# Kernel tuning notes

Hardware: AMD Instinct MI355X
Metric: run time of the kernel (lower is better)

The kernel has to match this reference:

```python
import jax, jax.numpy as jnp
import numpy as np

BUCKET_SIZE = 64  # init kwarg bucket_size
DIM = 64          # init kwarg dim (per-head dim, used for scaling)


def setup_inputs() -> dict:
    key = jax.random.key(0)
    kq, kk = jax.random.split(key)
    q = jax.random.normal(kq, (32, 8192, 64), dtype=jnp.float32)
    k = jax.random.normal(kk, (32, 8192, 64), dtype=jnp.float32)
    return {"q": q, "k": k}


def _cumavg(t):
    # cumulative average along the sequence axis (axis=1)
    r = jnp.arange(1, t.shape[1] + 1, dtype=t.dtype)
    return jnp.cumsum(t, axis=1) / r[None, :, None]


def reference(q, k):
    bh, n, d = q.shape
    buckets = n // BUCKET_SIZE
    kv_buckets = k.shape[1] // BUCKET_SIZE

    # bucket the cumulative averages: [bh, buckets, bucket_size, d]
    q_r = _cumavg(q).reshape(bh, buckets, BUCKET_SIZE, d)
    k_r = _cumavg(k).reshape(bh, kv_buckets, BUCKET_SIZE, d)

    sq = q_r[:, :, 0]                                   # [bh, buckets, d]
    sk = k_r.sum(axis=2)                                # [bh, kv_buckets, d]
    sk = jnp.pad(sk, ((0, 0), (1, 0), (0, 0)))          # pad one zero bucket row at front

    R = jnp.einsum('bie,bje->bij', sq, sk) * (DIM ** -0.5)  # [bh, buckets, kv_buckets+1]

    rows = jnp.arange(buckets)[:, None]
    cols = jnp.arange(kv_buckets + 1)[None, :]
    neg = -jnp.finfo(R.dtype).max
    # masked_fill: for row i, columns i+1..buckets set to -max (cols > rows)
    R = jnp.where(cols > rows, neg, R)
    R = jax.nn.softmax(R, axis=-1)
    # tril(diagonal=-1): keep entries with col < row
    R = jnp.where(cols < rows, R, jnp.zeros((), R.dtype))
    return R
```

## Files before the change

kernel.cpp:

```cpp
#include <hip/hip_runtime.h>
#include <cstddef>

constexpr int BH = 32;
constexpr int N  = 8192;
constexpr int D  = 64;
constexpr int BK = 64;
constexpr int NB = 128;
constexpr int NC = 129;

__global__ __launch_bounds__(256) void kA(const float* __restrict__ q,
                                          const float* __restrict__ k,
                                          float* __restrict__ qsum,
                                          float* __restrict__ ksum,
                                          float* __restrict__ kw,
                                          float* __restrict__ qfirst,
                                          float* __restrict__ W) {
  const int wv   = threadIdx.x >> 6;
  const int lane = threadIdx.x & 63;
  const int f    = lane & 15;
  const int r    = lane >> 4;
  const int j    = blockIdx.x * 4 + wv;
  const int b    = blockIdx.y;
  const int side = blockIdx.z;
  const int base = j * BK;
  const size_t ob = ((size_t)b * NB + j) * D;

  const float* src = (side == 0 ? q : k) + ((size_t)b * N + base) * D;
  const float4* s4 = (const float4*)src;

  if (side == 0) {
    float4 v[16];
#pragma unroll
    for (int p = 0; p < 16; ++p) v[p] = s4[(r * 16 + p) * 16 + f];

    float a[4] = {0, 0, 0, 0};
#pragma unroll
    for (int p = 0; p < 16; ++p) {
      a[0] += v[p].x; a[1] += v[p].y; a[2] += v[p].z; a[3] += v[p].w;
    }
#pragma unroll
    for (int c = 0; c < 4; ++c) {
      a[c] += __shfl_xor(a[c], 16, 64);
      a[c] += __shfl_xor(a[c], 32, 64);
    }
    if (r == 0) {
      ((float4*)(qsum + ob))[f] = make_float4(a[0], a[1], a[2], a[3]);
      ((float4*)(qfirst + ob))[f] = v[0];
    }
  } else {
    float4 v[16];
#pragma unroll
    for (int p = 0; p < 16; ++p) v[p] = s4[(r * 16 + 15 - p) * 16 + f];

    float ak[4] = {0, 0, 0, 0}, aw[4] = {0, 0, 0, 0};
    float wh = 0.0f;
#pragma unroll
    for (int p = 0; p < 16; ++p) {
      const int row = r * 16 + 15 - p;
      wh += 1.0f / (float)(base + row + 1);
      ak[0] += v[p].x; ak[1] += v[p].y; ak[2] += v[p].z; ak[3] += v[p].w;
      aw[0] += v[p].x * wh; aw[1] += v[p].y * wh;
      aw[2] += v[p].z * wh; aw[3] += v[p].w * wh;
    }

    const float w16 = __shfl_xor(wh, 16, 64);
    const float w32 = __shfl_xor(wh, 32, 64);
    const float w48 = __shfl_xor(wh, 48, 64);
    float TU = 0.0f;
    if ((r ^ 1) > r) TU += w16;
    if ((r ^ 2) > r) TU += w32;
    if ((r ^ 3) > r) TU += w48;
    const float Wfull = wh + w16 + w32 + w48;

#pragma unroll
    for (int c = 0; c < 4; ++c) aw[c] += TU * ak[c];
#pragma unroll
    for (int c = 0; c < 4; ++c) {
      ak[c] += __shfl_xor(ak[c], 16, 64); ak[c] += __shfl_xor(ak[c], 32, 64);
      aw[c] += __shfl_xor(aw[c], 16, 64); aw[c] += __shfl_xor(aw[c], 32, 64);
    }
    if (r == 0) {
      ((float4*)(ksum + ob))[f] = make_float4(ak[0], ak[1], ak[2], ak[3]);
      ((float4*)(kw   + ob))[f] = make_float4(aw[0], aw[1], aw[2], aw[3]);
      if (lane == 0 && b == 0) W[j] = Wfull;
    }
  }
}

__global__ __launch_bounds__(256) void kB(const float* __restrict__ qsum,
                                          const float* __restrict__ ksum,
                                          const float* __restrict__ kw,
                                          const float* __restrict__ qfirst,
                                          const float* __restrict__ W,
                                          float* __restrict__ sq,
                                          float* __restrict__ skp) {
  const int side = blockIdx.x;
  const int b    = blockIdx.y;
  const int tid  = threadIdx.x;
  const int d    = tid & 63;
  const int jg   = tid >> 6;

  __shared__ float buf[NB * D];
  __shared__ float tot[4 * D];
  __shared__ float Wl[NB];

  const float* src = (side == 0 ? qsum : ksum) + (size_t)b * NB * D;
  {
    const float4* g4 = (const float4*)src;
    float4* l4 = (float4*)buf;
    for (int u = tid; u < NB * D / 4; u += 256) l4[u] = g4[u];
    if (side == 1 && tid < NB) Wl[tid] = W[tid];
  }
  __syncthreads();

  float t0 = 0.0f;
  for (int jj = 0; jj < 32; ++jj) t0 += buf[(jg * 32 + jj) * D + d];
  tot[jg * D + d] = t0;
  __syncthreads();

  float pre = 0.0f;
  for (int g = 0; g < jg; ++g) pre += tot[g * D + d];

  if (side == 0) {
    for (int jj = 0; jj < 32; ++jj) {
      const int j = jg * 32 + jj;
      const size_t o = ((size_t)b * NB + j) * D + d;
      sq[o] = (pre + qfirst[o]) / (float)(j * BK + 1);
      pre += buf[j * D + d];
    }
  } else {
    if (tid < D) skp[(size_t)b * NC * D + tid] = 0.0f;
    for (int jj = 0; jj < 32; ++jj) {
      const int j = jg * 32 + jj;
      const size_t o = ((size_t)b * NB + j) * D + d;
      skp[((size_t)b * NC + j + 1) * D + d] = pre * Wl[j] + kw[o];
      pre += buf[j * D + d];
    }
  }
}

__global__ __launch_bounds__(256) void kC(const float* __restrict__ sq,
                                          const float* __restrict__ skp,
                                          float* __restrict__ out) {
  const int tile = blockIdx.x, b = blockIdx.y;
  const int tid = threadIdx.x;
  const int jp = tid & 63, rep = tid >> 6;
  const int T0 = tile * 8;
  const int rows = T0 + 8;

  __shared__ float skpS[NB * D];
  __shared__ float sqs[8 * D];

  {
    const float4* g4 = (const float4*)(skp + (size_t)b * NC * D);
    for (int u = tid; u < rows * 16; u += 256) {
      const int row = u >> 4, f = u & 15;
      ((float4*)skpS)[row * 16 + ((f + row) & 15)] = g4[u];
    }
    if (tid < 128)
      ((float4*)sqs)[tid] = ((const float4*)(sq + ((size_t)b * NB + T0) * D))[tid];
  }
  __syncthreads();

  float acc0[2] = {0, 0}, acc1[2] = {0, 0};
  const float4* sk4 = (const float4*)skpS;
  const float4* sq4 = (const float4*)sqs;
#pragma unroll
  for (int d4 = 0; d4 < 16; ++d4) {
    const int slot = (d4 + jp) & 15;
    const float4 k0 = sk4[jp * 16 + slot];
    const float4 k1 = sk4[(jp + 64) * 16 + slot];
#pragma unroll
    for (int ii = 0; ii < 2; ++ii) {
      const float4 s = sq4[(rep * 2 + ii) * 16 + d4];
      acc0[ii] += s.x * k0.x + s.y * k0.y + s.z * k0.z + s.w * k0.w;
      acc1[ii] += s.x * k1.x + s.y * k1.y + s.z * k1.z + s.w * k1.w;
    }
  }

#pragma unroll
  for (int ii = 0; ii < 2; ++ii) {
    const int i = T0 + rep * 2 + ii;
    const int j0 = jp, j1 = jp + 64;
    const float v0 = acc0[ii] * 0.125f, v1 = acc1[ii] * 0.125f;
    const bool val0 = (j0 <= i), val1 = (j1 <= i);
    float m = fmaxf(val0 ? v0 : -3.402823466e38f, val1 ? v1 : -3.402823466e38f);
#pragma unroll
    for (int s = 1; s < 64; s <<= 1) m = fmaxf(m, __shfl_xor(m, s, 64));
    const float e0 = val0 ? __expf(v0 - m) : 0.0f;
    const float e1 = val1 ? __expf(v1 - m) : 0.0f;
    float ss = e0 + e1;
#pragma unroll
    for (int s = 1; s < 64; s <<= 1) ss += __shfl_xor(ss, s, 64);
    const float rden = 1.0f / ss;
    float* orow = out + ((size_t)b * NB + i) * NC;
    orow[j0] = (j0 < i) ? e0 * rden : 0.0f;
    orow[j1] = (j1 < i) ? e1 * rden : 0.0f;
    if (jp == 0) orow[128] = 0.0f;
  }
}

extern "C" void kernel_launch(void* const* d_in, const int* in_sizes, int n_in,
                              void* d_out, int out_size, void* d_ws, size_t ws_size,
                              hipStream_t stream) {
  const float* q = (const float*)d_in[0];
  const float* k = (const float*)d_in[1];
  float* out = (float*)d_out;

  float* ws     = (float*)d_ws;
  float* qsum   = ws;
  float* ksum   = qsum   + (size_t)BH * NB * D;
  float* kw     = ksum   + (size_t)BH * NB * D;
  float* qfirst = kw     + (size_t)BH * NB * D;
  float* sq     = qfirst + (size_t)BH * NB * D;
  float* skp    = sq     + (size_t)BH * NB * D;
  float* W      = skp    + (size_t)BH * NC * D;

  kA<<<dim3(NB / 4, BH, 2), 256, 0, stream>>>(q, k, qsum, ksum, kw, qfirst, W);
  kB<<<dim3(2, BH), 256, 0, stream>>>(qsum, ksum, kw, qfirst, W, sq, skp);
  kC<<<dim3(16, BH), 256, 0, stream>>>(sq, skp, out);
}
```

Measured before the change: 160.6 us.

## Restructure bucket reduction kernel: one block per bucket handling both q and k

The first kernel now assigns one 256-thread block per (bucket, head) that loads both q and k rows, instead of one wavefront per bucket per side. The harmonic weight suffix sums are computed with a wave-level shuffle scan, and per-wave partials are combined through shared memory. The aim is more memory-level parallelism: each thread holds fewer float4 loads in flight and more blocks are spread across CUs. The cost is an extra shared-memory reduction and a barrier per block.

```diff
diff --git a/kernel.cpp b/kernel.cpp
--- a/kernel.cpp
+++ b/kernel.cpp
@@ -8,82 +8,74 @@
 constexpr int NB = 128;
 constexpr int NC = 129;
 
-__global__ __launch_bounds__(256) void kA(const float* __restrict__ q,
-                                          const float* __restrict__ k,
-                                          float* __restrict__ qsum,
-                                          float* __restrict__ ksum,
-                                          float* __restrict__ kw,
-                                          float* __restrict__ qfirst,
-                                          float* __restrict__ W) {
-  const int wv   = threadIdx.x >> 6;
-  const int lane = threadIdx.x & 63;
-  const int f    = lane & 15;
-  const int r    = lane >> 4;
-  const int j    = blockIdx.x * 4 + wv;
-  const int b    = blockIdx.y;
-  const int side = blockIdx.z;
+__global__ __launch_bounds__(256, 1) void kA(const float* __restrict__ q,
+                                             const float* __restrict__ k,
+                                             float* __restrict__ qsum,
+                                             float* __restrict__ ksum,
+                                             float* __restrict__ kw,
+                                             float* __restrict__ qfirst,
+                                             float* __restrict__ W) {
+  const int j = blockIdx.x, b = blockIdx.y;
+  const int tid  = threadIdx.x;
+  const int f    = tid & 15;
+  const int rr   = tid >> 4;
+  const int w    = tid >> 6;
+  const int lane = tid & 63;
   const int base = j * BK;
   const size_t ob = ((size_t)b * NB + j) * D;
 
-  const float* src = (side == 0 ? q : k) + ((size_t)b * N + base) * D;
-  const float4* s4 = (const float4*)src;
-
-  if (side == 0) {
-    float4 v[16];
-#pragma unroll
-    for (int p = 0; p < 16; ++p) v[p] = s4[(r * 16 + p) * 16 + f];
-
-    float a[4] = {0, 0, 0, 0};
-#pragma unroll
-    for (int p = 0; p < 16; ++p) {
-      a[0] += v[p].x; a[1] += v[p].y; a[2] += v[p].z; a[3] += v[p].w;
-    }
-#pragma unroll
-    for (int c = 0; c < 4; ++c) {
-      a[c] += __shfl_xor(a[c], 16, 64);
-      a[c] += __shfl_xor(a[c], 32, 64);
-    }
-    if (r == 0) {
-      ((float4*)(qsum + ob))[f] = make_float4(a[0], a[1], a[2], a[3]);
-      ((float4*)(qfirst + ob))[f] = v[0];
-    }
-  } else {
-    float4 v[16];
-#pragma unroll
-    for (int p = 0; p < 16; ++p) v[p] = s4[(r * 16 + 15 - p) * 16 + f];
-
-    float ak[4] = {0, 0, 0, 0}, aw[4] = {0, 0, 0, 0};
-    float wh = 0.0f;
-#pragma unroll
-    for (int p = 0; p < 16; ++p) {
-      const int row = r * 16 + 15 - p;
-      wh += 1.0f / (float)(base + row + 1);
-      ak[0] += v[p].x; ak[1] += v[p].y; ak[2] += v[p].z; ak[3] += v[p].w;
-      aw[0] += v[p].x * wh; aw[1] += v[p].y * wh;
-      aw[2] += v[p].z * wh; aw[3] += v[p].w * wh;
-    }
-
-    const float w16 = __shfl_xor(wh, 16, 64);
-    const float w32 = __shfl_xor(wh, 32, 64);
-    const float w48 = __shfl_xor(wh, 48, 64);
-    float TU = 0.0f;
-    if ((r ^ 1) > r) TU += w16;
-    if ((r ^ 2) > r) TU += w32;
-    if ((r ^ 3) > r) TU += w48;
-    const float Wfull = wh + w16 + w32 + w48;
-
-#pragma unroll
-    for (int c = 0; c < 4; ++c) aw[c] += TU * ak[c];
-#pragma unroll
-    for (int c = 0; c < 4; ++c) {
-      ak[c] += __shfl_xor(ak[c], 16, 64); ak[c] += __shfl_xor(ak[c], 32, 64);
-      aw[c] += __shfl_xor(aw[c], 16, 64); aw[c] += __shfl_xor(aw[c], 32, 64);
-    }
-    if (r == 0) {
-      ((float4*)(ksum + ob))[f] = make_float4(ak[0], ak[1], ak[2], ak[3]);
-      ((float4*)(kw   + ob))[f] = make_float4(aw[0], aw[1], aw[2], aw[3]);
-      if (lane == 0 && b == 0) W[j] = Wfull;
-    }
+  const float4* q4 = (const float4*)(q + ((size_t)b * N + base) * D);
+  const float4* k4 = (const float4*)(k + ((size_t)b * N + base) * D);
+
+  float4 vq[4], vk[4];
+#pragma unroll
+  for (int p = 0; p < 4; ++p) vq[p] = q4[(16 * p + rr) * 16 + f];
+#pragma unroll
+  for (int p = 0; p < 4; ++p) vk[p] = k4[(16 * p + rr) * 16 + f];
+
+  float x = 1.0f / (float)(base + lane + 1);
+#pragma unroll
+  for (int s = 1; s < 64; s <<= 1) {
+    const float y = __shfl_down(x, s, 64);
+    if (lane + s < 64) x += y;
+  }
+  float tw[4];
+#pragma unroll
+  for (int p = 0; p < 4; ++p) tw[p] = __shfl(x, 16 * p + rr, 64);
+
+  float aq[4] = {0, 0, 0, 0}, ak[4] = {0, 0, 0, 0}, aw[4] = {0, 0, 0, 0};
+#pragma unroll
+  for (int p = 0; p < 4; ++p) {
+    aq[0] += vq[p].x; aq[1] += vq[p].y; aq[2] += vq[p].z; aq[3] += vq[p].w;
+    ak[0] += vk[p].x; ak[1] += vk[p].y; ak[2] += vk[p].z; ak[3] += vk[p].w;
+    aw[0] += vk[p].x * tw[p]; aw[1] += vk[p].y * tw[p];
+    aw[2] += vk[p].z * tw[p]; aw[3] += vk[p].w * tw[p];
+  }
+
+#pragma unroll
+  for (int c = 0; c < 4; ++c) {
+    aq[c] += __shfl_xor(aq[c], 16, 64); aq[c] += __shfl_xor(aq[c], 32, 64);
+    ak[c] += __shfl_xor(ak[c], 16, 64); ak[c] += __shfl_xor(ak[c], 32, 64);
+    aw[c] += __shfl_xor(aw[c], 16, 64); aw[c] += __shfl_xor(aw[c], 32, 64);
+  }
+
+  __shared__ float red[3][4][D];
+  if (lane < 16) {
+    ((float4*)&red[0][w][0])[f] = make_float4(aq[0], aq[1], aq[2], aq[3]);
+    ((float4*)&red[1][w][0])[f] = make_float4(ak[0], ak[1], ak[2], ak[3]);
+    ((float4*)&red[2][w][0])[f] = make_float4(aw[0], aw[1], aw[2], aw[3]);
+  }
+  if (rr == 0) {
+    ((float4*)(qfirst + ob))[f] = vq[0];
+  }
+  if (tid == 0 && b == 0) W[j] = x;
+  __syncthreads();
+
+  if (tid < 192) {
+    const int arr = tid >> 6, d = tid & 63;
+    const float s = red[arr][0][d] + red[arr][1][d] + red[arr][2][d] + red[arr][3][d];
+    float* dst = (arr == 0) ? qsum : (arr == 1) ? ksum : kw;
+    dst[ob + d] = s;
   }
 }
 
@@ -216,7 +208,7 @@
   float* skp    = sq     + (size_t)BH * NB * D;
   float* W      = skp    + (size_t)BH * NC * D;
 
-  kA<<<dim3(NB / 4, BH, 2), 256, 0, stream>>>(q, k, qsum, ksum, kw, qfirst, W);
+  kA<<<dim3(NB, BH), 256, 0, stream>>>(q, k, qsum, ksum, kw, qfirst, W);
   kB<<<dim3(2, BH), 256, 0, stream>>>(qsum, ksum, kw, qfirst, W, sq, skp);
   kC<<<dim3(16, BH), 256, 0, stream>>>(sq, skp, out);
 }
```

After: 156.7 us. -2.4%, faster.
